# Performance work log

Hardware: AMD Instinct MI355X
Metric: run time of the kernel (lower is better)

Reference implementation:

```python
import jax, jax.numpy as jnp
import numpy as np

B, N, H = 2, 2048, 1024
NUM_HEADS = 16
HEAD_DIM = H // NUM_HEADS
SCALE = HEAD_DIM ** -0.5


def setup_inputs() -> dict:
    key = jax.random.key(0)
    k1, k2, k3, k4 = jax.random.split(key, 4)
    s = 0.02
    return {
        "x": jax.random.normal(k1, (B, N, H), dtype=jnp.float32),
        "x2": jax.random.normal(k2, (B, N, H), dtype=jnp.float32),
        "Wqkv": jax.random.normal(k3, (H, 3 * H), dtype=jnp.float32) * s,
        "Wout": jax.random.normal(k4, (H, H), dtype=jnp.float32) * s,
        "bout": jnp.zeros((H,), dtype=jnp.float32),
    }


def _split_qkv(t):
    # t: [B, N, 3H] -> [3, B, h, N, d]
    b, n, _ = t.shape
    t = t.reshape(b, n, 3, NUM_HEADS, HEAD_DIM)
    return jnp.transpose(t, (2, 0, 3, 1, 4))


def reference(x, x2, Wqkv, Wout, bout):
    # shared qkv projection applied to both streams (bias=False)
    qkv2 = _split_qkv(x2 @ Wqkv)  # k, v from x2
    k, v = qkv2[1], qkv2[2]       # [B, h, N2, d]
    qkv1 = _split_qkv(x @ Wqkv)   # q from x
    q = qkv1[0]                   # [B, h, N, d]

    att = jax.nn.softmax(jnp.einsum("bhxd,bhyd->bhxy", q, k) * SCALE, axis=-1)
    out = jnp.einsum("bhxy,bhyd->bhxd", att, v)        # [B, h, N, d]
    out = jnp.transpose(out, (0, 2, 1, 3)).reshape(x.shape[0], x.shape[1], -1)
    return out @ Wout + bout
```

## Files before the change

### kernel.cpp

```cpp
#include <hip/hip_runtime.h>

#define B_ 2
#define N_ 2048
#define H_ 1024
#define NH_ 16
#define D_ 64

typedef _Float16 f16;
typedef _Float16 f16x4 __attribute__((ext_vector_type(4)));
typedef _Float16 f16x8 __attribute__((ext_vector_type(8)));
typedef float f32x4 __attribute__((ext_vector_type(4)));

#define MFMA16(a, b, c) __builtin_amdgcn_mfma_f32_16x16x32_f16((a), (b), (c), 0, 0, 0)

__global__ __launch_bounds__(256) void transw(
    const float* __restrict__ W, f16* __restrict__ Wt, int rows, int ncols) {
  const int cb = blockIdx.x * 64;
  const int kb = blockIdx.y * 64;
  const int t = threadIdx.x;
  __shared__ f16 T[64][72];
  {
    const int k = t >> 2, c0 = (t & 3) * 16;
    const float* wp = W + (size_t)(kb + k) * ncols + cb + c0;
    float4 w0 = ((const float4*)wp)[0];
    float4 w1 = ((const float4*)wp)[1];
    float4 w2 = ((const float4*)wp)[2];
    float4 w3 = ((const float4*)wp)[3];
    T[c0 + 0][k] = (f16)w0.x;  T[c0 + 1][k] = (f16)w0.y;
    T[c0 + 2][k] = (f16)w0.z;  T[c0 + 3][k] = (f16)w0.w;
    T[c0 + 4][k] = (f16)w1.x;  T[c0 + 5][k] = (f16)w1.y;
    T[c0 + 6][k] = (f16)w1.z;  T[c0 + 7][k] = (f16)w1.w;
    T[c0 + 8][k] = (f16)w2.x;  T[c0 + 9][k] = (f16)w2.y;
    T[c0 + 10][k] = (f16)w2.z; T[c0 + 11][k] = (f16)w2.w;
    T[c0 + 12][k] = (f16)w3.x; T[c0 + 13][k] = (f16)w3.y;
    T[c0 + 14][k] = (f16)w3.z; T[c0 + 15][k] = (f16)w3.w;
  }
  __syncthreads();
  {
    const int c = t >> 2, k0 = (t & 3) * 16;
    f16* op = Wt + (size_t)(cb + c) * rows + kb + k0;
    *(f16x8*)(op + 0) = *(const f16x8*)(&T[c][k0]);
    *(f16x8*)(op + 8) = *(const f16x8*)(&T[c][k0 + 8]);
  }
}

__global__ __launch_bounds__(256) void transv(
    const f16* __restrict__ V, f16* __restrict__ Vt) {
  const int nb = blockIdx.x * 64;
  const int bh = blockIdx.y;
  const int t = threadIdx.x;
  __shared__ f16 T[64][72];
  {
    const int n = t >> 2, d0 = (t & 3) * 16;
    const f16* vp = V + ((size_t)bh * N_ + nb + n) * D_ + d0;
    f16x8 v0 = *(const f16x8*)(vp);
    f16x8 v1 = *(const f16x8*)(vp + 8);
#pragma unroll
    for (int i = 0; i < 8; ++i) T[d0 + i][n] = v0[i];
#pragma unroll
    for (int i = 0; i < 8; ++i) T[d0 + 8 + i][n] = v1[i];
  }
  __syncthreads();
  {
    const int d = t >> 2, n0 = (t & 3) * 16;
    f16* op = Vt + ((size_t)bh * D_ + d) * N_ + nb + n0;
    *(f16x8*)(op + 0) = *(const f16x8*)(&T[d][n0]);
    *(f16x8*)(op + 8) = *(const f16x8*)(&T[d][n0 + 8]);
  }
}

__global__ __launch_bounds__(256) void qkv_mfma(
    const float* __restrict__ x, const float* __restrict__ x2,
    const f16* __restrict__ Wt, f16* __restrict__ Qo,
    f16* __restrict__ Ko, f16* __restrict__ Vo) {
  const int cb = blockIdx.x * 128;
  const int rb = blockIdx.y * 128;
  const int t = threadIdx.x;
  const int lane = t & 63, wid = t >> 6;
  const int quad = lane >> 4, n16 = lane & 15;
  const int wm = wid >> 1, wn = wid & 1;

  const float* __restrict__ A = (cb < H_) ? x : x2;
  const int seg = cb >> 10;
  const float qscale = (seg == 0) ? 0.125f : 1.0f;
  f16* __restrict__ outp = (seg == 0) ? Qo : (seg == 1 ? Ko : Vo);

  __shared__ f16 As[128 * 40];
  __shared__ f16 Bs[128 * 40];

  f32x4 acc[4][4];
#pragma unroll
  for (int i = 0; i < 4; ++i)
#pragma unroll
    for (int j = 0; j < 4; ++j) acc[i][j] = (f32x4){0.f, 0.f, 0.f, 0.f};

  const int ar = t >> 1, ak = (t & 1) * 16;
  const int bn = t >> 1, bk = (t & 1) * 16;

  for (int kt = 0; kt < H_; kt += 32) {
    __syncthreads();
    const float* ap = A + (size_t)(rb + ar) * H_ + kt + ak;
    float4 a0 = ((const float4*)ap)[0];
    float4 a1 = ((const float4*)ap)[1];
    float4 a2 = ((const float4*)ap)[2];
    float4 a3 = ((const float4*)ap)[3];
    f16x8 pk0, pk1;
    pk0[0] = (f16)a0.x; pk0[1] = (f16)a0.y; pk0[2] = (f16)a0.z; pk0[3] = (f16)a0.w;
    pk0[4] = (f16)a1.x; pk0[5] = (f16)a1.y; pk0[6] = (f16)a1.z; pk0[7] = (f16)a1.w;
    pk1[0] = (f16)a2.x; pk1[1] = (f16)a2.y; pk1[2] = (f16)a2.z; pk1[3] = (f16)a2.w;
    pk1[4] = (f16)a3.x; pk1[5] = (f16)a3.y; pk1[6] = (f16)a3.z; pk1[7] = (f16)a3.w;
    *(f16x8*)(&As[ar * 40 + ak]) = pk0;
    *(f16x8*)(&As[ar * 40 + ak + 8]) = pk1;
    const f16* wp = Wt + (size_t)(cb + bn) * H_ + kt + bk;
    *(f16x8*)(&Bs[bn * 40 + bk]) = *(const f16x8*)(wp);
    *(f16x8*)(&Bs[bn * 40 + bk + 8]) = *(const f16x8*)(wp + 8);
    __syncthreads();

    f16x8 af[4], bf[4];
#pragma unroll
    for (int mt = 0; mt < 4; ++mt)
      af[mt] = *(const f16x8*)(&As[(wm * 64 + mt * 16 + n16) * 40 + quad * 8]);
#pragma unroll
    for (int nt = 0; nt < 4; ++nt)
      bf[nt] = *(const f16x8*)(&Bs[(wn * 64 + nt * 16 + n16) * 40 + quad * 8]);
#pragma unroll
    for (int mt = 0; mt < 4; ++mt)
#pragma unroll
      for (int nt = 0; nt < 4; ++nt)
        acc[mt][nt] = MFMA16(af[mt], bf[nt], acc[mt][nt]);
  }

#pragma unroll
  for (int mt = 0; mt < 4; ++mt)
#pragma unroll
    for (int nt = 0; nt < 4; ++nt)
#pragma unroll
      for (int r = 0; r < 4; ++r) {
        int grow = rb + wm * 64 + mt * 16 + quad * 4 + r;
        int gcol = cb + wn * 64 + nt * 16 + n16;
        int bb = grow >> 11, nn = grow & 2047;
        int hh = (gcol >> 6) & 15, dd = gcol & 63;
        outp[(((size_t)(bb * NH_ + hh)) * N_ + nn) * D_ + dd] =
            (f16)(acc[mt][nt][r] * qscale);
      }
}

__global__ __launch_bounds__(256) void attn2(
    const f16* __restrict__ Q, const f16* __restrict__ K,
    const f16* __restrict__ Vt, f16* __restrict__ AO) {
  const int bh = blockIdx.y;
  const int b = bh >> 4, h = bh & 15;
  const int qb = blockIdx.x * 128;
  const int t = threadIdx.x;
  const int lane = t & 63, wid = t >> 6;
  const int quad = lane >> 4, n16 = lane & 15;

  const f16* __restrict__ Qp = Q + (size_t)bh * N_ * D_;
  const f16* __restrict__ Kp = K + (size_t)bh * N_ * D_;
  const f16* __restrict__ Vp = Vt + (size_t)bh * D_ * N_;

  __shared__ f16 Ks[64 * 72];
  __shared__ f16 Vs[64 * 72];
  __shared__ f16 Ps[4][32 * 72];

  f16x8 qf[2][2];
#pragma unroll
  for (int qc = 0; qc < 2; ++qc) {
    const f16* qp = Qp + (size_t)(qb + wid * 32 + qc * 16 + n16) * D_ + quad * 8;
    qf[qc][0] = *(const f16x8*)(qp);
    qf[qc][1] = *(const f16x8*)(qp + 32);
  }

  f32x4 o[2][4];
#pragma unroll
  for (int i = 0; i < 2; ++i)
#pragma unroll
    for (int j = 0; j < 4; ++j) o[i][j] = (f32x4){0.f, 0.f, 0.f, 0.f};
  float lsum[2] = {0.f, 0.f};

  const int sr = t >> 2, sc = (t & 3) * 16;
  const f16* kg = Kp + (size_t)sr * D_ + sc;
  const f16* vg = Vp + (size_t)sr * N_ + sc;

  f16x8 ka0 = *(const f16x8*)(kg);
  f16x8 ka1 = *(const f16x8*)(kg + 8);
  f16x8 va0 = *(const f16x8*)(vg);
  f16x8 va1 = *(const f16x8*)(vg + 8);

  for (int kt = 0; kt < N_; kt += 64) {
    *(f16x8*)(&Ks[sr * 72 + sc]) = ka0;
    *(f16x8*)(&Ks[sr * 72 + sc + 8]) = ka1;
    *(f16x8*)(&Vs[sr * 72 + sc]) = va0;
    *(f16x8*)(&Vs[sr * 72 + sc + 8]) = va1;
    __syncthreads();

    if (kt + 64 < N_) {
      const f16* kg2 = kg + (size_t)(kt + 64) * D_;
      const f16* vg2 = vg + (kt + 64);
      ka0 = *(const f16x8*)(kg2);
      ka1 = *(const f16x8*)(kg2 + 8);
      va0 = *(const f16x8*)(vg2);
      va1 = *(const f16x8*)(vg2 + 8);
    }

    f32x4 s[4][2];
#pragma unroll
    for (int kc = 0; kc < 4; ++kc) {
      const f16x8 kf0 = *(const f16x8*)(&Ks[(kc * 16 + n16) * 72 + quad * 8]);
      const f16x8 kf1 = *(const f16x8*)(&Ks[(kc * 16 + n16) * 72 + 32 + quad * 8]);
#pragma unroll
      for (int qc = 0; qc < 2; ++qc) {
        f32x4 sv = (f32x4){0.f, 0.f, 0.f, 0.f};
        sv = MFMA16(kf0, qf[qc][0], sv);
        sv = MFMA16(kf1, qf[qc][1], sv);
        s[kc][qc] = sv;
      }
    }

    f16* __restrict__ pw = Ps[wid];
#pragma unroll
    for (int qc = 0; qc < 2; ++qc) {
      float ls = 0.f;
#pragma unroll
      for (int kc = 0; kc < 4; ++kc) {
        f16x4 pk;
#pragma unroll
        for (int r = 0; r < 4; ++r) {
          float p = __expf(s[kc][qc][r]);
          ls += p;
          pk[r] = (f16)p;
        }
        *(f16x4*)(&pw[(qc * 16 + n16) * 72 + kc * 16 + quad * 4]) = pk;
      }
      lsum[qc] += ls;
    }

    f16x8 vf[4][2];
#pragma unroll
    for (int dt = 0; dt < 4; ++dt) {
      vf[dt][0] = *(const f16x8*)(&Vs[(dt * 16 + n16) * 72 + quad * 8]);
      vf[dt][1] = *(const f16x8*)(&Vs[(dt * 16 + n16) * 72 + 32 + quad * 8]);
    }
#pragma unroll
    for (int mq = 0; mq < 2; ++mq) {
      const f16x8 pa0 = *(const f16x8*)(&pw[(mq * 16 + n16) * 72 + quad * 8]);
      const f16x8 pa1 = *(const f16x8*)(&pw[(mq * 16 + n16) * 72 + 32 + quad * 8]);
#pragma unroll
      for (int dt = 0; dt < 4; ++dt) {
        o[mq][dt] = MFMA16(pa0, vf[dt][0], o[mq][dt]);
        o[mq][dt] = MFMA16(pa1, vf[dt][1], o[mq][dt]);
      }
    }
    __syncthreads();
  }

#pragma unroll
  for (int qc = 0; qc < 2; ++qc) {
    lsum[qc] += __shfl_xor(lsum[qc], 16);
    lsum[qc] += __shfl_xor(lsum[qc], 32);
  }

#pragma unroll
  for (int mq = 0; mq < 2; ++mq)
#pragma unroll
    for (int r = 0; r < 4; ++r) {
      float inv = 1.0f / __shfl(lsum[mq], quad * 4 + r);
      int nrow = qb + wid * 32 + mq * 16 + quad * 4 + r;
      f16* aop = AO + ((size_t)(b * N_ + nrow)) * H_ + h * 64;
#pragma unroll
      for (int dt = 0; dt < 4; ++dt)
        aop[dt * 16 + n16] = (f16)(o[mq][dt][r] * inv);
    }
}

__global__ __launch_bounds__(256) void out_mfma(
    const f16* __restrict__ A, const f16* __restrict__ Wt,
    const float* __restrict__ bias, float* __restrict__ out) {
  const int cb = blockIdx.x * 128;
  const int rb = blockIdx.y * 128;
  const int t = threadIdx.x;
  const int lane = t & 63, wid = t >> 6;
  const int quad = lane >> 4, n16 = lane & 15;
  const int wm = wid >> 1, wn = wid & 1;

  __shared__ f16 As[128 * 40];
  __shared__ f16 Bs[128 * 40];

  f32x4 acc[4][4];
#pragma unroll
  for (int i = 0; i < 4; ++i)
#pragma unroll
    for (int j = 0; j < 4; ++j) acc[i][j] = (f32x4){0.f, 0.f, 0.f, 0.f};

  const int ar = t >> 1, ak = (t & 1) * 16;

  for (int kt = 0; kt < H_; kt += 32) {
    __syncthreads();
    const f16* ap = A + (size_t)(rb + ar) * H_ + kt + ak;
    *(f16x8*)(&As[ar * 40 + ak]) = *(const f16x8*)(ap);
    *(f16x8*)(&As[ar * 40 + ak + 8]) = *(const f16x8*)(ap + 8);
    const f16* wp = Wt + (size_t)(cb + ar) * H_ + kt + ak;
    *(f16x8*)(&Bs[ar * 40 + ak]) = *(const f16x8*)(wp);
    *(f16x8*)(&Bs[ar * 40 + ak + 8]) = *(const f16x8*)(wp + 8);
    __syncthreads();

    f16x8 af[4], bf[4];
#pragma unroll
    for (int mt = 0; mt < 4; ++mt)
      af[mt] = *(const f16x8*)(&As[(wm * 64 + mt * 16 + n16) * 40 + quad * 8]);
#pragma unroll
    for (int nt = 0; nt < 4; ++nt)
      bf[nt] = *(const f16x8*)(&Bs[(wn * 64 + nt * 16 + n16) * 40 + quad * 8]);
#pragma unroll
    for (int mt = 0; mt < 4; ++mt)
#pragma unroll
      for (int nt = 0; nt < 4; ++nt)
        acc[mt][nt] = MFMA16(af[mt], bf[nt], acc[mt][nt]);
  }

#pragma unroll
  for (int nt = 0; nt < 4; ++nt) {
    int gcol = cb + wn * 64 + nt * 16 + n16;
    float bv = bias[gcol];
#pragma unroll
    for (int mt = 0; mt < 4; ++mt)
#pragma unroll
      for (int r = 0; r < 4; ++r) {
        int grow = rb + wm * 64 + mt * 16 + quad * 4 + r;
        out[(size_t)grow * H_ + gcol] = acc[mt][nt][r] + bv;
      }
  }
}

extern "C" void kernel_launch(void* const* d_in, const int* in_sizes, int n_in,
                              void* d_out, int out_size, void* d_ws, size_t ws_size,
                              hipStream_t stream) {
  const float* x    = (const float*)d_in[0];
  const float* x2   = (const float*)d_in[1];
  const float* Wqkv = (const float*)d_in[2];
  const float* Wout = (const float*)d_in[3];
  const float* bout = (const float*)d_in[4];
  float* out = (float*)d_out;

  const size_t per = (size_t)B_ * NH_ * N_ * D_;
  f16* Qw    = (f16*)d_ws;
  f16* Kw    = Qw + per;
  f16* Vw    = Kw + per;
  f16* Vtw   = Vw + per;
  f16* AO    = Vtw + per;
  f16* WqkvT = AO + per;
  f16* WoutT = WqkvT + (size_t)3072 * 1024;

  transw<<<dim3(48, 16), 256, 0, stream>>>(Wqkv, WqkvT, H_, 3 * H_);
  transw<<<dim3(16, 16), 256, 0, stream>>>(Wout, WoutT, H_, H_);
  qkv_mfma<<<dim3(24, 32), 256, 0, stream>>>(x, x2, WqkvT, Qw, Kw, Vw);
  transv<<<dim3(32, 32), 256, 0, stream>>>(Vw, Vtw);
  attn2<<<dim3(16, 32), 256, 0, stream>>>(Qw, Kw, Vtw, AO);
  out_mfma<<<dim3(8, 32), 256, 0, stream>>>(AO, WoutT, bout, out);
}
```

Measured before the change: 233.3 us.

## Use direct global-to-LDS loads with swizzled layouts and pre-convert inputs to fp16

Replaces register-staged shared-memory fills in the QKV GEMM, attention and output GEMM with global_load_lds async copies into XOR-swizzled unpadded tiles. Adds a separate kernel converting x and x2 to fp16 so the GEMM loads fp16 directly. Folds log2(e) into the Q scale and uses exp2, and remaps grids to 1D with row-fastest ordering. It drops the register prefetch in attention and adds an extra conversion pass over the inputs.

Result: faster. 205.3 us (-12.0%).

```diff
diff --git a/kernel.cpp b/kernel.cpp
--- a/kernel.cpp
+++ b/kernel.cpp
@@ -13,10 +13,29 @@
 
 #define MFMA16(a, b, c) __builtin_amdgcn_mfma_f32_16x16x32_f16((a), (b), (c), 0, 0, 0)
 
+__device__ __forceinline__ void cp16(void* lds, const void* g) {
+  __builtin_amdgcn_global_load_lds(
+      (const __attribute__((address_space(1))) void*)g,
+      (__attribute__((address_space(3))) void*)lds, 16, 0, 0);
+}
+
+__global__ __launch_bounds__(256) void convf16(
+    const float* __restrict__ a, const float* __restrict__ b,
+    f16* __restrict__ ao, f16* __restrict__ bo) {
+  const size_t i = ((size_t)blockIdx.x * 256 + threadIdx.x) * 8;
+  const float* __restrict__ src = (blockIdx.y == 0) ? a : b;
+  f16* __restrict__ dst = (blockIdx.y == 0) ? ao : bo;
+  float4 v0 = ((const float4*)(src + i))[0];
+  float4 v1 = ((const float4*)(src + i))[1];
+  f16x8 o;
+  o[0] = (f16)v0.x; o[1] = (f16)v0.y; o[2] = (f16)v0.z; o[3] = (f16)v0.w;
+  o[4] = (f16)v1.x; o[5] = (f16)v1.y; o[6] = (f16)v1.z; o[7] = (f16)v1.w;
+  *(f16x8*)(dst + i) = o;
+}
+
 __global__ __launch_bounds__(256) void transw(
     const float* __restrict__ W, f16* __restrict__ Wt, int rows, int ncols) {
-  const int cb = blockIdx.x * 64;
-  const int kb = blockIdx.y * 64;
+  const int cb = blockIdx.x * 64, kb = blockIdx.y * 64;
   const int t = threadIdx.x;
   __shared__ f16 T[64][72];
   {
@@ -46,8 +65,7 @@
 
 __global__ __launch_bounds__(256) void transv(
     const f16* __restrict__ V, f16* __restrict__ Vt) {
-  const int nb = blockIdx.x * 64;
-  const int bh = blockIdx.y;
+  const int nb = blockIdx.x * 64, bh = blockIdx.y;
   const int t = threadIdx.x;
   __shared__ f16 T[64][72];
   {
@@ -70,23 +88,24 @@
 }
 
 __global__ __launch_bounds__(256) void qkv_mfma(
-    const float* __restrict__ x, const float* __restrict__ x2,
+    const f16* __restrict__ Xc, const f16* __restrict__ X2c,
     const f16* __restrict__ Wt, f16* __restrict__ Qo,
     f16* __restrict__ Ko, f16* __restrict__ Vo) {
-  const int cb = blockIdx.x * 128;
-  const int rb = blockIdx.y * 128;
+  const int bid = blockIdx.x;
+  const int rb = (bid & 31) * 128;
+  const int cb = (bid >> 5) * 128;
   const int t = threadIdx.x;
   const int lane = t & 63, wid = t >> 6;
   const int quad = lane >> 4, n16 = lane & 15;
   const int wm = wid >> 1, wn = wid & 1;
 
-  const float* __restrict__ A = (cb < H_) ? x : x2;
+  const f16* __restrict__ A = (cb < H_) ? Xc : X2c;
   const int seg = cb >> 10;
-  const float qscale = (seg == 0) ? 0.125f : 1.0f;
+  const float qscale = (seg == 0) ? 0.125f * 1.44269504f : 1.0f;
   f16* __restrict__ outp = (seg == 0) ? Qo : (seg == 1 ? Ko : Vo);
 
-  __shared__ f16 As[128 * 40];
-  __shared__ f16 Bs[128 * 40];
+  __shared__ f16 As[128 * 32];
+  __shared__ f16 Bs[128 * 32];
 
   f32x4 acc[4][4];
 #pragma unroll
@@ -94,35 +113,39 @@
 #pragma unroll
     for (int j = 0; j < 4; ++j) acc[i][j] = (f32x4){0.f, 0.f, 0.f, 0.f};
 
-  const int ar = t >> 1, ak = (t & 1) * 16;
-  const int bn = t >> 1, bk = (t & 1) * 16;
+  int srow0 = wid * 16 + (lane >> 2);
+  int srow1 = 64 + srow0;
+  int gl0 = ((lane & 3) ^ ((srow0 >> 1) & 3)) * 8;
+  int gl1 = ((lane & 3) ^ ((srow1 >> 1) & 3)) * 8;
+  const f16* gA0 = A + (size_t)(rb + srow0) * H_ + gl0;
+  const f16* gA1 = A + (size_t)(rb + srow1) * H_ + gl1;
+  const f16* gB0 = Wt + (size_t)(cb + srow0) * H_ + gl0;
+  const f16* gB1 = Wt + (size_t)(cb + srow1) * H_ + gl1;
+  f16* lA0 = &As[wid * 512];
+  f16* lA1 = &As[2048 + wid * 512];
+  f16* lB0 = &Bs[wid * 512];
+  f16* lB1 = &Bs[2048 + wid * 512];
+
+  const int fsw = (quad ^ ((n16 >> 1) & 3)) * 8;
+  int aoff[4], boff[4];
+#pragma unroll
+  for (int i = 0; i < 4; ++i) {
+    aoff[i] = (wm * 64 + i * 16 + n16) * 32 + fsw;
+    boff[i] = (wn * 64 + i * 16 + n16) * 32 + fsw;
+  }
 
   for (int kt = 0; kt < H_; kt += 32) {
     __syncthreads();
-    const float* ap = A + (size_t)(rb + ar) * H_ + kt + ak;
-    float4 a0 = ((const float4*)ap)[0];
-    float4 a1 = ((const float4*)ap)[1];
-    float4 a2 = ((const float4*)ap)[2];
-    float4 a3 = ((const float4*)ap)[3];
-    f16x8 pk0, pk1;
-    pk0[0] = (f16)a0.x; pk0[1] = (f16)a0.y; pk0[2] = (f16)a0.z; pk0[3] = (f16)a0.w;
-    pk0[4] = (f16)a1.x; pk0[5] = (f16)a1.y; pk0[6] = (f16)a1.z; pk0[7] = (f16)a1.w;
-    pk1[0] = (f16)a2.x; pk1[1] = (f16)a2.y; pk1[2] = (f16)a2.z; pk1[3] = (f16)a2.w;
-    pk1[4] = (f16)a3.x; pk1[5] = (f16)a3.y; pk1[6] = (f16)a3.z; pk1[7] = (f16)a3.w;
-    *(f16x8*)(&As[ar * 40 + ak]) = pk0;
-    *(f16x8*)(&As[ar * 40 + ak + 8]) = pk1;
-    const f16* wp = Wt + (size_t)(cb + bn) * H_ + kt + bk;
-    *(f16x8*)(&Bs[bn * 40 + bk]) = *(const f16x8*)(wp);
-    *(f16x8*)(&Bs[bn * 40 + bk + 8]) = *(const f16x8*)(wp + 8);
+    cp16(lA0, gA0); cp16(lA1, gA1);
+    cp16(lB0, gB0); cp16(lB1, gB1);
+    gA0 += 32; gA1 += 32; gB0 += 32; gB1 += 32;
     __syncthreads();
 
     f16x8 af[4], bf[4];
 #pragma unroll
-    for (int mt = 0; mt < 4; ++mt)
-      af[mt] = *(const f16x8*)(&As[(wm * 64 + mt * 16 + n16) * 40 + quad * 8]);
-#pragma unroll
-    for (int nt = 0; nt < 4; ++nt)
-      bf[nt] = *(const f16x8*)(&Bs[(wn * 64 + nt * 16 + n16) * 40 + quad * 8]);
+    for (int mt = 0; mt < 4; ++mt) af[mt] = *(const f16x8*)(&As[aoff[mt]]);
+#pragma unroll
+    for (int nt = 0; nt < 4; ++nt) bf[nt] = *(const f16x8*)(&Bs[boff[nt]]);
 #pragma unroll
     for (int mt = 0; mt < 4; ++mt)
 #pragma unroll
@@ -159,8 +182,8 @@
   const f16* __restrict__ Kp = K + (size_t)bh * N_ * D_;
   const f16* __restrict__ Vp = Vt + (size_t)bh * D_ * N_;
 
-  __shared__ f16 Ks[64 * 72];
-  __shared__ f16 Vs[64 * 72];
+  __shared__ f16 Ks[64 * 64];
+  __shared__ f16 Vs[64 * 64];
   __shared__ f16 Ps[4][32 * 72];
 
   f16x8 qf[2][2];
@@ -178,36 +201,34 @@
     for (int j = 0; j < 4; ++j) o[i][j] = (f32x4){0.f, 0.f, 0.f, 0.f};
   float lsum[2] = {0.f, 0.f};
 
-  const int sr = t >> 2, sc = (t & 3) * 16;
-  const f16* kg = Kp + (size_t)sr * D_ + sc;
-  const f16* vg = Vp + (size_t)sr * N_ + sc;
-
-  f16x8 ka0 = *(const f16x8*)(kg);
-  f16x8 ka1 = *(const f16x8*)(kg + 8);
-  f16x8 va0 = *(const f16x8*)(vg);
-  f16x8 va1 = *(const f16x8*)(vg + 8);
+  int srow0 = wid * 8 + (lane >> 3);
+  int srow1 = 32 + srow0;
+  int gl0 = ((lane & 7) ^ (srow0 & 7)) * 8;
+  int gl1 = ((lane & 7) ^ (srow1 & 7)) * 8;
+  const f16* gK0 = Kp + (size_t)srow0 * D_ + gl0;
+  const f16* gK1 = Kp + (size_t)srow1 * D_ + gl1;
+  const f16* gV0 = Vp + (size_t)srow0 * N_ + gl0;
+  const f16* gV1 = Vp + (size_t)srow1 * N_ + gl1;
+  f16* lK0 = &Ks[wid * 512];
+  f16* lK1 = &Ks[2048 + wid * 512];
+  f16* lV0 = &Vs[wid * 512];
+  f16* lV1 = &Vs[2048 + wid * 512];
+
+  const int fs0 = (quad ^ (n16 & 7)) * 8;
+  const int fs1 = ((quad + 4) ^ (n16 & 7)) * 8;
 
   for (int kt = 0; kt < N_; kt += 64) {
-    *(f16x8*)(&Ks[sr * 72 + sc]) = ka0;
-    *(f16x8*)(&Ks[sr * 72 + sc + 8]) = ka1;
-    *(f16x8*)(&Vs[sr * 72 + sc]) = va0;
-    *(f16x8*)(&Vs[sr * 72 + sc + 8]) = va1;
-    __syncthreads();
-
-    if (kt + 64 < N_) {
-      const f16* kg2 = kg + (size_t)(kt + 64) * D_;
-      const f16* vg2 = vg + (kt + 64);
-      ka0 = *(const f16x8*)(kg2);
-      ka1 = *(const f16x8*)(kg2 + 8);
-      va0 = *(const f16x8*)(vg2);
-      va1 = *(const f16x8*)(vg2 + 8);
-    }
+    __syncthreads();
+    cp16(lK0, gK0); cp16(lK1, gK1);
+    cp16(lV0, gV0); cp16(lV1, gV1);
+    gK0 += 64 * D_; gK1 += 64 * D_; gV0 += 64; gV1 += 64;
+    __syncthreads();
 
     f32x4 s[4][2];
 #pragma unroll
     for (int kc = 0; kc < 4; ++kc) {
-      const f16x8 kf0 = *(const f16x8*)(&Ks[(kc * 16 + n16) * 72 + quad * 8]);
-      const f16x8 kf1 = *(const f16x8*)(&Ks[(kc * 16 + n16) * 72 + 32 + quad * 8]);
+      const f16x8 kf0 = *(const f16x8*)(&Ks[(kc * 16 + n16) * 64 + fs0]);
+      const f16x8 kf1 = *(const f16x8*)(&Ks[(kc * 16 + n16) * 64 + fs1]);
 #pragma unroll
       for (int qc = 0; qc < 2; ++qc) {
         f32x4 sv = (f32x4){0.f, 0.f, 0.f, 0.f};
@@ -226,7 +247,7 @@
         f16x4 pk;
 #pragma unroll
         for (int r = 0; r < 4; ++r) {
-          float p = __expf(s[kc][qc][r]);
+          float p = __builtin_amdgcn_exp2f(s[kc][qc][r]);
           ls += p;
           pk[r] = (f16)p;
         }
@@ -238,8 +259,8 @@
     f16x8 vf[4][2];
 #pragma unroll
     for (int dt = 0; dt < 4; ++dt) {
-      vf[dt][0] = *(const f16x8*)(&Vs[(dt * 16 + n16) * 72 + quad * 8]);
-      vf[dt][1] = *(const f16x8*)(&Vs[(dt * 16 + n16) * 72 + 32 + quad * 8]);
+      vf[dt][0] = *(const f16x8*)(&Vs[(dt * 16 + n16) * 64 + fs0]);
+      vf[dt][1] = *(const f16x8*)(&Vs[(dt * 16 + n16) * 64 + fs1]);
     }
 #pragma unroll
     for (int mq = 0; mq < 2; ++mq) {
@@ -251,7 +272,6 @@
         o[mq][dt] = MFMA16(pa1, vf[dt][1], o[mq][dt]);
       }
     }
-    __syncthreads();
   }
 
 #pragma unroll
@@ -276,15 +296,16 @@
 __global__ __launch_bounds__(256) void out_mfma(
     const f16* __restrict__ A, const f16* __restrict__ Wt,
     const float* __restrict__ bias, float* __restrict__ out) {
-  const int cb = blockIdx.x * 128;
-  const int rb = blockIdx.y * 128;
+  const int bid = blockIdx.x;
+  const int rb = (bid & 31) * 128;
+  const int cb = (bid >> 5) * 128;
   const int t = threadIdx.x;
   const int lane = t & 63, wid = t >> 6;
   const int quad = lane >> 4, n16 = lane & 15;
   const int wm = wid >> 1, wn = wid & 1;
 
-  __shared__ f16 As[128 * 40];
-  __shared__ f16 Bs[128 * 40];
+  __shared__ f16 As[128 * 32];
+  __shared__ f16 Bs[128 * 32];
 
   f32x4 acc[4][4];
 #pragma unroll
@@ -292,25 +313,39 @@
 #pragma unroll
     for (int j = 0; j < 4; ++j) acc[i][j] = (f32x4){0.f, 0.f, 0.f, 0.f};
 
-  const int ar = t >> 1, ak = (t & 1) * 16;
+  int srow0 = wid * 16 + (lane >> 2);
+  int srow1 = 64 + srow0;
+  int gl0 = ((lane & 3) ^ ((srow0 >> 1) & 3)) * 8;
+  int gl1 = ((lane & 3) ^ ((srow1 >> 1) & 3)) * 8;
+  const f16* gA0 = A + (size_t)(rb + srow0) * H_ + gl0;
+  const f16* gA1 = A + (size_t)(rb + srow1) * H_ + gl1;
+  const f16* gB0 = Wt + (size_t)(cb + srow0) * H_ + gl0;
+  const f16* gB1 = Wt + (size_t)(cb + srow1) * H_ + gl1;
+  f16* lA0 = &As[wid * 512];
+  f16* lA1 = &As[2048 + wid * 512];
+  f16* lB0 = &Bs[wid * 512];
+  f16* lB1 = &Bs[2048 + wid * 512];
+
+  const int fsw = (quad ^ ((n16 >> 1) & 3)) * 8;
+  int aoff[4], boff[4];
+#pragma unroll
+  for (int i = 0; i < 4; ++i) {
+    aoff[i] = (wm * 64 + i * 16 + n16) * 32 + fsw;
+    boff[i] = (wn * 64 + i * 16 + n16) * 32 + fsw;
+  }
 
   for (int kt = 0; kt < H_; kt += 32) {
     __syncthreads();
-    const f16* ap = A + (size_t)(rb + ar) * H_ + kt + ak;
-    *(f16x8*)(&As[ar * 40 + ak]) = *(const f16x8*)(ap);
-    *(f16x8*)(&As[ar * 40 + ak + 8]) = *(const f16x8*)(ap + 8);
-    const f16* wp = Wt + (size_t)(cb + ar) * H_ + kt + ak;
-    *(f16x8*)(&Bs[ar * 40 + ak]) = *(const f16x8*)(wp);
-    *(f16x8*)(&Bs[ar * 40 + ak + 8]) = *(const f16x8*)(wp + 8);
+    cp16(lA0, gA0); cp16(lA1, gA1);
+    cp16(lB0, gB0); cp16(lB1, gB1);
+    gA0 += 32; gA1 += 32; gB0 += 32; gB1 += 32;
     __syncthreads();
 
     f16x8 af[4], bf[4];
 #pragma unroll
-    for (int mt = 0; mt < 4; ++mt)
-      af[mt] = *(const f16x8*)(&As[(wm * 64 + mt * 16 + n16) * 40 + quad * 8]);
-#pragma unroll
-    for (int nt = 0; nt < 4; ++nt)
-      bf[nt] = *(const f16x8*)(&Bs[(wn * 64 + nt * 16 + n16) * 40 + quad * 8]);
+    for (int mt = 0; mt < 4; ++mt) af[mt] = *(const f16x8*)(&As[aoff[mt]]);
+#pragma unroll
+    for (int nt = 0; nt < 4; ++nt) bf[nt] = *(const f16x8*)(&Bs[boff[nt]]);
 #pragma unroll
     for (int mt = 0; mt < 4; ++mt)
 #pragma unroll
@@ -343,7 +378,9 @@
   float* out = (float*)d_out;
 
   const size_t per = (size_t)B_ * NH_ * N_ * D_;
-  f16* Qw    = (f16*)d_ws;
+  f16* Xc    = (f16*)d_ws;
+  f16* X2c   = Xc + per;
+  f16* Qw    = X2c + per;
   f16* Kw    = Qw + per;
   f16* Vw    = Kw + per;
   f16* Vtw   = Vw + per;
@@ -351,10 +388,11 @@
   f16* WqkvT = AO + per;
   f16* WoutT = WqkvT + (size_t)3072 * 1024;
 
+  convf16<<<dim3(2048, 2), 256, 0, stream>>>(x, x2, Xc, X2c);
   transw<<<dim3(48, 16), 256, 0, stream>>>(Wqkv, WqkvT, H_, 3 * H_);
   transw<<<dim3(16, 16), 256, 0, stream>>>(Wout, WoutT, H_, H_);
-  qkv_mfma<<<dim3(24, 32), 256, 0, stream>>>(x, x2, WqkvT, Qw, Kw, Vw);
+  qkv_mfma<<<dim3(768), 256, 0, stream>>>(Xc, X2c, WqkvT, Qw, Kw, Vw);
   transv<<<dim3(32, 32), 256, 0, stream>>>(Vw, Vtw);
   attn2<<<dim3(16, 32), 256, 0, stream>>>(Qw, Kw, Vtw, AO);
-  out_mfma<<<dim3(8, 32), 256, 0, stream>>>(AO, WoutT, bout, out);
-}
+  out_mfma<<<dim3(256), 256, 0, stream>>>(AO, WoutT, bout, out);
+}
```
